# Kernel optimization log

Hardware: AMD Instinct MI355X
Metric: run time of the kernel (lower is better)

Reference implementation:

```python
import jax, jax.numpy as jnp
import numpy as np

N_AGENTS = 8

def _nearest(x, codebook):
    # x: [N, D], codebook: [K, D] -> indices [N]
    # squared L2 distance via expansion; argmin over codebook axis
    d2 = (jnp.sum(x * x, axis=1, keepdims=True)
          - 2.0 * x @ codebook.T
          + jnp.sum(codebook * codebook, axis=1)[None, :])  # [N, K]
    return jnp.argmin(d2, axis=1)

def setup_inputs() -> dict:
    key = jax.random.key(0)
    ks = jax.random.split(key, 16)
    s = 0.02
    H, D_in, R, K, S = 512, 256, 64, 256, 512
    inp = {
        "inputs": jax.random.normal(ks[0], (131072, D_in), jnp.float32),
        "W0": jax.random.normal(ks[1], (D_in, H), jnp.float32) * s,
        "b0": jnp.zeros((H,), jnp.float32),
        "W1": jax.random.normal(ks[2], (H, H), jnp.float32) * s,
        "b1": jnp.zeros((H,), jnp.float32),
        "W2": jax.random.normal(ks[3], (H, R), jnp.float32) * s,
        "b2": jnp.zeros((R,), jnp.float32),
        "codebook": jax.random.normal(ks[4], (K, R), jnp.float32),
        "W3": jax.random.normal(ks[5], (R, H), jnp.float32) * s,
        "b3": jnp.zeros((H,), jnp.float32),
        "W4": jax.random.normal(ks[6], (N_AGENTS * H, H), jnp.float32) * s,
        "b4": jnp.zeros((H,), jnp.float32),
        "W5": jax.random.normal(ks[7], (H, S), jnp.float32) * s,
        "b5": jnp.zeros((S,), jnp.float32),
    }
    return inp

def reference(inputs, W0, b0, W1, b1, W2, b2, codebook, W3, b3, W4, b4, W5, b5):
    # encode: fc2(relu(fc1(relu(fc0(x)))))
    h = jax.nn.relu(inputs @ W0 + b0)
    h = jax.nn.relu(h @ W1 + b1)
    z_e = h @ W2 + b2  # [N, role_dim]

    # emb(z_e, weight_sg=True): straight-through to z_e, codebook detached
    idx1 = _nearest(z_e, codebook)
    z_q_raw = jnp.take(codebook, idx1, axis=0)
    z_q = z_e + jax.lax.stop_gradient(z_q_raw - z_e)

    # emb(z_e.detach()): grad flows to codebook only (gather -> scatter-add vjp)
    z_e_sg = jax.lax.stop_gradient(z_e)
    idx2 = _nearest(z_e_sg, codebook)
    role_emb = jnp.take(codebook, idx2, axis=0)

    # decode
    rec = jax.nn.relu(z_q @ W3 + b3).reshape(-1, N_AGENTS * W3.shape[1])
    rec = jax.nn.relu(rec @ W4 + b4)
    recon = rec @ W5 + b5  # [N/n_agents, state_dim]
    return recon, z_e, role_emb
```

## Files before the change

kernel.cpp:

```cpp
#include <hip/hip_runtime.h>
#include <hip/hip_bf16.h>
#include <cstddef>

__device__ __forceinline__ unsigned short f2bf(float f) {
    union { float f; unsigned int u; } v; v.f = f;
    unsigned int r = (v.u + 0x7fffu + ((v.u >> 16) & 1u)) >> 16;
    return (unsigned short)r;
}

typedef __bf16    bf16x8 __attribute__((ext_vector_type(8)));
typedef float     f32x4  __attribute__((ext_vector_type(4)));
typedef _Float16  f16x8  __attribute__((ext_vector_type(8)));

#define SPLIT_SCALE 2.44140625e-4f

typedef const __attribute__((address_space(1))) void cglb_t;
typedef __attribute__((address_space(3))) void lds_t;

__device__ __forceinline__ void fsplit(float v, _Float16& hi, _Float16& lo) {
    hi = (_Float16)v;
    lo = (_Float16)((v - (float)hi) * 4096.0f);
}

__device__ __forceinline__ int swz4(int r) { return (r & 3) ^ ((r >> 2) & 3); }

template<int K>
__global__ __launch_bounds__(256, 3)
void gemm_split7(const _Float16* __restrict__ Ahi, const _Float16* __restrict__ Alo,
                 const _Float16* __restrict__ Bhi, const _Float16* __restrict__ Blo,
                 const float* __restrict__ bias,
                 _Float16* __restrict__ Chi, _Float16* __restrict__ Clo,
                 int M, int N)
{
    constexpr int BK = 32;
    constexpr int NS = K / BK;

    __shared__ alignas(16) _Float16 SA[2][2][128 * 32];
    __shared__ alignas(16) _Float16 SB[2][2][64 * 32];

    const int tid  = threadIdx.x;
    const int lane = tid & 63;
    const int w    = tid >> 6;

    int bx = blockIdx.x, by = blockIdx.y;
    {
        const int gx = gridDim.x, nwg = gx * gridDim.y;
        if ((nwg & 7) == 0) {
            int d = bx + by * gx;
            int L = (d & 7) * (nwg >> 3) + (d >> 3);
            bx = L % gx; by = L / gx;
        }
    }
    const int bm = by * 128;
    const int bn = bx * 64;

    f32x4 acc0[2][4], acc1[2][4];
#pragma unroll
    for (int m = 0; m < 2; ++m)
#pragma unroll
        for (int n = 0; n < 4; ++n) {
            acc0[m][n] = (f32x4){0.f, 0.f, 0.f, 0.f};
            acc1[m][n] = (f32x4){0.f, 0.f, 0.f, 0.f};
        }

    auto stage = [&](int buf, int k0) {
#pragma unroll
        for (int pl = 0; pl < 2; ++pl) {
            const _Float16* src = pl ? Alo : Ahi;
#pragma unroll
            for (int j = 0; j < 2; ++j) {
                const int p16 = (w * 2 + j) * 64 + lane;
                const int r   = p16 >> 2;
                const int c   = (p16 & 3) ^ swz4(r);
                const _Float16* g = src + (size_t)(bm + r) * K + k0 + c * 8;
                __builtin_amdgcn_global_load_lds((cglb_t*)g,
                    (lds_t*)&SA[buf][pl][p16 * 8], 16, 0, 0);
            }
            const _Float16* srcB = pl ? Blo : Bhi;
            const int p16b = w * 64 + lane;
            const int rb   = p16b >> 2;
            const int cb   = (p16b & 3) ^ swz4(rb);
            const _Float16* gB = srcB + (size_t)(bn + rb) * K + k0 + cb * 8;
            __builtin_amdgcn_global_load_lds((cglb_t*)gB,
                (lds_t*)&SB[buf][pl][p16b * 8], 16, 0, 0);
        }
    };

    stage(0, 0);
    __syncthreads();

    const int g   = lane >> 4;
    const int r15 = lane & 15;

#pragma unroll
    for (int s = 0; s < NS; ++s) {
        const int p = s & 1;
        if (s + 1 < NS) stage(p ^ 1, (s + 1) * BK);

        f16x8 ah[2], al[2];
#pragma unroll
        for (int m = 0; m < 2; ++m) {
            const int R = w * 32 + m * 16 + r15;
            const int a16 = R * 4 + (g ^ swz4(R));
            ah[m] = *reinterpret_cast<const f16x8*>(&SA[p][0][a16 * 8]);
            al[m] = *reinterpret_cast<const f16x8*>(&SA[p][1][a16 * 8]);
        }
#pragma unroll
        for (int n = 0; n < 4; ++n) {
            const int rB = n * 16 + r15;
            const int b16 = rB * 4 + (g ^ swz4(rB));
            const f16x8 bh = *reinterpret_cast<const f16x8*>(&SB[p][0][b16 * 8]);
            const f16x8 bl = *reinterpret_cast<const f16x8*>(&SB[p][1][b16 * 8]);
#pragma unroll
            for (int m = 0; m < 2; ++m)
                acc0[m][n] = __builtin_amdgcn_mfma_f32_16x16x32_f16(
                    ah[m], bh, acc0[m][n], 0, 0, 0);
#pragma unroll
            for (int m = 0; m < 2; ++m)
                acc1[m][n] = __builtin_amdgcn_mfma_f32_16x16x32_f16(
                    ah[m], bl, acc1[m][n], 0, 0, 0);
#pragma unroll
            for (int m = 0; m < 2; ++m)
                acc1[m][n] = __builtin_amdgcn_mfma_f32_16x16x32_f16(
                    al[m], bh, acc1[m][n], 0, 0, 0);
        }
        __syncthreads();
    }

#pragma unroll
    for (int m = 0; m < 2; ++m)
#pragma unroll
        for (int n = 0; n < 4; ++n) {
            const int col = bn + n * 16 + r15;
            const float bv = bias[col];
#pragma unroll
            for (int q = 0; q < 4; ++q) {
                const int row = bm + w * 32 + m * 16 + (lane >> 4) * 4 + q;
                float v = acc0[m][n][q] + SPLIT_SCALE * acc1[m][n][q] + bv;
                v = fmaxf(v, 0.f);
                _Float16 hi, lo; fsplit(v, hi, lo);
                Chi[(size_t)row * N + col] = hi;
                Clo[(size_t)row * N + col] = lo;
            }
        }
}

template<bool RELU, bool OUT_BF16>
__global__ __launch_bounds__(256, 3)
void gemm_bt7(const unsigned short* __restrict__ A,
              const unsigned short* __restrict__ Bt,
              const float* __restrict__ bias,
              void* __restrict__ Cv, int M, int N, int K)
{
    constexpr int BK = 32;

    __shared__ alignas(16) unsigned short SA[2][128 * 32];
    __shared__ alignas(16) unsigned short SB[2][128 * 32];

    const int tid  = threadIdx.x;
    const int lane = tid & 63;
    const int w    = tid >> 6;
    const int wr   = (w >> 1) * 64;
    const int wc   = (w & 1) * 64;

    int bx = blockIdx.x, by = blockIdx.y;
    {
        const int gx = gridDim.x, nwg = gx * gridDim.y;
        if ((nwg & 7) == 0) {
            int d = bx + by * gx;
            int L = (d & 7) * (nwg >> 3) + (d >> 3);
            bx = L % gx; by = L / gx;
        }
    }
    const int bm = by * 128;
    const int bn = bx * 128;

    f32x4 acc[4][4];
#pragma unroll
    for (int m = 0; m < 4; ++m)
#pragma unroll
        for (int n = 0; n < 4; ++n) acc[m][n] = (f32x4){0.f, 0.f, 0.f, 0.f};

    auto stage = [&](int buf, int k0) {
#pragma unroll
        for (int j = 0; j < 2; ++j) {
            const int p16 = (w * 2 + j) * 64 + lane;
            const int r   = p16 >> 2;
            const int c   = (p16 & 3) ^ swz4(r);
            const unsigned short* gA = A + (size_t)(bm + r) * K + k0 + c * 8;
            __builtin_amdgcn_global_load_lds((cglb_t*)gA,
                (lds_t*)&SA[buf][p16 * 8], 16, 0, 0);
            const unsigned short* gB = Bt + (size_t)(bn + r) * K + k0 + c * 8;
            __builtin_amdgcn_global_load_lds((cglb_t*)gB,
                (lds_t*)&SB[buf][p16 * 8], 16, 0, 0);
        }
    };

    stage(0, 0);
    __syncthreads();

    const int g   = lane >> 4;
    const int r15 = lane & 15;
    const int NS  = K / BK;

    for (int s = 0; s < NS; ++s) {
        const int p = s & 1;
        if (s + 1 < NS) stage(p ^ 1, (s + 1) * BK);

        bf16x8 af[4], bf[4];
#pragma unroll
        for (int m = 0; m < 4; ++m) {
            const int R = wr + m * 16 + r15;
            const int a16 = R * 4 + (g ^ swz4(R));
            af[m] = *reinterpret_cast<const bf16x8*>(&SA[p][a16 * 8]);
        }
#pragma unroll
        for (int n = 0; n < 4; ++n) {
            const int RB = wc + n * 16 + r15;
            const int b16 = RB * 4 + (g ^ swz4(RB));
            bf[n] = *reinterpret_cast<const bf16x8*>(&SB[p][b16 * 8]);
        }
#pragma unroll
        for (int m = 0; m < 4; ++m)
#pragma unroll
            for (int n = 0; n < 4; ++n)
                acc[m][n] = __builtin_amdgcn_mfma_f32_16x16x32_bf16(
                    af[m], bf[n], acc[m][n], 0, 0, 0);
        __syncthreads();
    }

#pragma unroll
    for (int m = 0; m < 4; ++m)
#pragma unroll
        for (int n = 0; n < 4; ++n) {
            const int col = bn + wc + n * 16 + r15;
            const float bv = bias[col];
#pragma unroll
            for (int q = 0; q < 4; ++q) {
                const int row = bm + wr + m * 16 + (lane >> 4) * 4 + q;
                float v = acc[m][n][q] + bv;
                if (RELU) v = fmaxf(v, 0.f);
                if (OUT_BF16)
                    reinterpret_cast<unsigned short*>(Cv)[(size_t)row * N + col] = f2bf(v);
                else
                    reinterpret_cast<float*>(Cv)[(size_t)row * N + col] = v;
            }
        }
}

__global__ __launch_bounds__(256)
void gemm_ze_mfma(const _Float16* __restrict__ Ahi, const _Float16* __restrict__ Alo,
                  const _Float16* __restrict__ Bhi, const _Float16* __restrict__ Blo,
                  const float* __restrict__ bias, float* __restrict__ C, int M)
{
    constexpr int K = 512, N = 64;
    const int tid  = threadIdx.x;
    const int lane = tid & 63;
    const int w    = tid >> 6;
    const int wr   = (w >> 1) * 64;
    const int wc   = (w & 1) * 32;
    const int bm   = blockIdx.x * 128;

    f32x4 acc0[4][2], acc1[4][2];
#pragma unroll
    for (int m = 0; m < 4; ++m)
#pragma unroll
        for (int n = 0; n < 2; ++n) {
            acc0[m][n] = (f32x4){0.f, 0.f, 0.f, 0.f};
            acc1[m][n] = (f32x4){0.f, 0.f, 0.f, 0.f};
        }

    const int arow = bm + wr + (lane & 15);
    const int kgrp = (lane >> 4) * 8;

#pragma unroll
    for (int ks = 0; ks < K / 32; ++ks) {
        const int k0 = ks * 32 + kgrp;
        f16x8 ah[4], al[4];
#pragma unroll
        for (int m = 0; m < 4; ++m) {
            const size_t ga = (size_t)(arow + m * 16) * K + k0;
            ah[m] = *reinterpret_cast<const f16x8*>(Ahi + ga);
            al[m] = *reinterpret_cast<const f16x8*>(Alo + ga);
        }
#pragma unroll
        for (int n = 0; n < 2; ++n) {
            const size_t gb = (size_t)(wc + n * 16 + (lane & 15)) * K + k0;
            const f16x8 bh = *reinterpret_cast<const f16x8*>(Bhi + gb);
            const f16x8 bl = *reinterpret_cast<const f16x8*>(Blo + gb);
#pragma unroll
            for (int m = 0; m < 4; ++m)
                acc0[m][n] = __builtin_amdgcn_mfma_f32_16x16x32_f16(
                    ah[m], bh, acc0[m][n], 0, 0, 0);
#pragma unroll
            for (int m = 0; m < 4; ++m)
                acc1[m][n] = __builtin_amdgcn_mfma_f32_16x16x32_f16(
                    ah[m], bl, acc1[m][n], 0, 0, 0);
#pragma unroll
            for (int m = 0; m < 4; ++m)
                acc1[m][n] = __builtin_amdgcn_mfma_f32_16x16x32_f16(
                    al[m], bh, acc1[m][n], 0, 0, 0);
        }
    }

#pragma unroll
    for (int m = 0; m < 4; ++m)
#pragma unroll
        for (int n = 0; n < 2; ++n) {
            const int col = wc + n * 16 + (lane & 15);
            const float bv = bias[col];
#pragma unroll
            for (int q = 0; q < 4; ++q) {
                const int row = bm + wr + m * 16 + (lane >> 4) * 4 + q;
                C[(size_t)row * N + col] = acc0[m][n][q] + SPLIT_SCALE * acc1[m][n][q] + bv;
            }
        }
}

#define VQ_EPS 1e-3f
__global__ __launch_bounds__(512)
void vq_mfma(const float* __restrict__ Z, const float* __restrict__ CB,
             const _Float16* __restrict__ Chi, const _Float16* __restrict__ Clo,
             float* __restrict__ OUT, unsigned short* __restrict__ ZQB)
{
    __shared__ float  ccf[256];
    __shared__ double ccd[256];
    __shared__ float  xxf[128];
    __shared__ double xxd[128];
    __shared__ float  redv[4][128];
    __shared__ int    redi[4][128];
    __shared__ float  bv1s[128];
    __shared__ int    bis[128];
    __shared__ int    cand[128][16];
    __shared__ int    ncand[128];
    __shared__ int    fullflag[128];
    __shared__ int    flaglist[128];
    __shared__ int    nflag;

    const int tid  = threadIdx.x;
    const int lane = tid & 63;
    const int w    = tid >> 6;
    const int wr   = (w >> 2) * 64;
    const int wc   = (w & 3) * 64;
    const int bm   = blockIdx.x * 128;

    if (tid == 0) nflag = 0;
    if (tid < 256) {
        const float4* c4 = reinterpret_cast<const float4*>(CB + (size_t)tid * 64);
        double cc = 0.0;
#pragma unroll
        for (int v = 0; v < 16; ++v) {
            float4 f = c4[v];
            cc = fma((double)f.x, (double)f.x, cc);
            cc = fma((double)f.y, (double)f.y, cc);
            cc = fma((double)f.z, (double)f.z, cc);
            cc = fma((double)f.w, (double)f.w, cc);
        }
        ccd[tid] = cc; ccf[tid] = (float)cc;
    }
    if (tid < 128) {
        const float4* z4 = reinterpret_cast<const float4*>(Z + (size_t)(bm + tid) * 64);
        double xx = 0.0;
#pragma unroll
        for (int v = 0; v < 16; ++v) {
            float4 f = z4[v];
            xx = fma((double)f.x, (double)f.x, xx);
            xx = fma((double)f.y, (double)f.y, xx);
            xx = fma((double)f.z, (double)f.z, xx);
            xx = fma((double)f.w, (double)f.w, xx);
        }
        xxd[tid] = xx; xxf[tid] = (float)xx;
        ncand[tid] = 0; fullflag[tid] = 0;
    }
    __syncthreads();

    f32x4 acc0[4][4], acc1[4][4];
#pragma unroll
    for (int m = 0; m < 4; ++m)
#pragma unroll
        for (int n = 0; n < 4; ++n) {
            acc0[m][n] = (f32x4){0.f, 0.f, 0.f, 0.f};
            acc1[m][n] = (f32x4){0.f, 0.f, 0.f, 0.f};
        }

    const int arow = bm + wr + (lane & 15);
    const int kgrp = (lane >> 4) * 8;

#pragma unroll
    for (int ks = 0; ks < 2; ++ks) {
        const int k0 = ks * 32 + kgrp;
        f16x8 ah[4], al[4];
#pragma unroll
        for (int m = 0; m < 4; ++m) {
            const float* src = Z + (size_t)(arow + m * 16) * 64 + k0;
            float4 v0 = *reinterpret_cast<const float4*>(src);
            float4 v1 = *reinterpret_cast<const float4*>(src + 4);
            float vv[8] = {v0.x, v0.y, v0.z, v0.w, v1.x, v1.y, v1.z, v1.w};
            f16x8 hh, ll;
#pragma unroll
            for (int j = 0; j < 8; ++j) {
                _Float16 hi, lo; fsplit(vv[j], hi, lo);
                hh[j] = hi; ll[j] = lo;
            }
            ah[m] = hh; al[m] = ll;
        }
#pragma unroll
        for (int n = 0; n < 4; ++n) {
            const size_t gb = (size_t)(wc + n * 16 + (lane & 15)) * 64 + k0;
            const f16x8 bh = *reinterpret_cast<const f16x8*>(Chi + gb);
            const f16x8 bl = *reinterpret_cast<const f16x8*>(Clo + gb);
#pragma unroll
            for (int m = 0; m < 4; ++m)
                acc0[m][n] = __builtin_amdgcn_mfma_f32_16x16x32_f16(
                    ah[m], bh, acc0[m][n], 0, 0, 0);
#pragma unroll
            for (int m = 0; m < 4; ++m)
                acc1[m][n] = __builtin_amdgcn_mfma_f32_16x16x32_f16(
                    ah[m], bl, acc1[m][n], 0, 0, 0);
#pragma unroll
            for (int m = 0; m < 4; ++m)
                acc1[m][n] = __builtin_amdgcn_mfma_f32_16x16x32_f16(
                    al[m], bh, acc1[m][n], 0, 0, 0);
        }
    }

#pragma unroll
    for (int m = 0; m < 4; ++m)
#pragma unroll
        for (int n = 0; n < 4; ++n) {
            const int col = wc + n * 16 + (lane & 15);
            const float cf = ccf[col];
#pragma unroll
            for (int q = 0; q < 4; ++q) {
                const int rl = wr + m * 16 + (lane >> 4) * 4 + q;
                float dot = acc0[m][n][q] + SPLIT_SCALE * acc1[m][n][q];
                acc0[m][n][q] = (xxf[rl] - 2.0f * dot) + cf;
            }
        }

    float bvr[4][4]; int bir[4][4];
#pragma unroll
    for (int m = 0; m < 4; ++m)
#pragma unroll
        for (int q = 0; q < 4; ++q) {
            float bv = 3.4e38f; int bi = 0;
#pragma unroll
            for (int n = 0; n < 4; ++n) {
                const int col = wc + n * 16 + (lane & 15);
                const float v = acc0[m][n][q];
                if (v < bv || (v == bv && col < bi)) { bv = v; bi = col; }
            }
            bvr[m][q] = bv; bir[m][q] = bi;
        }
#pragma unroll
    for (int mask = 1; mask < 16; mask <<= 1) {
#pragma unroll
        for (int m = 0; m < 4; ++m)
#pragma unroll
            for (int q = 0; q < 4; ++q) {
                float ov = __shfl_xor(bvr[m][q], mask);
                int   oi = __shfl_xor(bir[m][q], mask);
                if (ov < bvr[m][q] || (ov == bvr[m][q] && oi < bir[m][q])) {
                    bvr[m][q] = ov; bir[m][q] = oi;
                }
            }
    }
    if ((lane & 15) == 0) {
#pragma unroll
        for (int m = 0; m < 4; ++m)
#pragma unroll
            for (int q = 0; q < 4; ++q) {
                const int rl = wr + m * 16 + (lane >> 4) * 4 + q;
                redv[w & 3][rl] = bvr[m][q];
                redi[w & 3][rl] = bir[m][q];
            }
    }
    __syncthreads();

    if (tid < 128) {
        float bv = 3.4e38f; int bi = 0;
#pragma unroll
        for (int nw = 0; nw < 4; ++nw) {
            float v = redv[nw][tid];
            if (v < bv) { bv = v; bi = redi[nw][tid]; }
        }
        bv1s[tid] = bv; bis[tid] = bi;
    }
    __syncthreads();

#pragma unroll
    for (int m = 0; m < 4; ++m)
#pragma unroll
        for (int q = 0; q < 4; ++q) {
            const int rl = wr + m * 16 + (lane >> 4) * 4 + q;
            const float thr = bv1s[rl] + VQ_EPS;
#pragma unroll
            for (int n = 0; n < 4; ++n) {
                const int col = wc + n * 16 + (lane & 15);
                if (acc0[m][n][q] <= thr) {
                    int s = atomicAdd(&ncand[rl], 1);
                    if (s < 16) cand[rl][s] = col;
                    else        fullflag[rl] = 1;
                }
            }
        }
    __syncthreads();

    if (tid < 128) {
        const int nc_ = ncand[tid] < 16 ? ncand[tid] : 16;
        if (nc_ > 1 && !fullflag[tid]) {
            const float4* z4p = reinterpret_cast<const float4*>(Z + (size_t)(bm + tid) * 64);
            const double xx = xxd[tid];
            double best = 1.0e300; int bi = 256;
            for (int s = 0; s < nc_; ++s) {
                const int e = cand[tid][s];
                const float4* c4p = reinterpret_cast<const float4*>(CB + (size_t)e * 64);
                double dot = 0.0;
#pragma unroll
                for (int v = 0; v < 16; ++v) {
                    float4 zf = z4p[v], cf4 = c4p[v];
                    dot = fma((double)zf.x, (double)cf4.x, dot);
                    dot = fma((double)zf.y, (double)cf4.y, dot);
                    dot = fma((double)zf.z, (double)cf4.z, dot);
                    dot = fma((double)zf.w, (double)cf4.w, dot);
                }
                double d2x = (xx - 2.0 * dot) + ccd[e];
                if (d2x < best || (d2x == best && e < bi)) { best = d2x; bi = e; }
            }
            bis[tid] = bi;
        }
        if (fullflag[tid]) {
            int s = atomicAdd(&nflag, 1);
            flaglist[s] = tid;
        }
    }
    __syncthreads();

    for (int fi = w; fi < nflag; fi += 8) {
        const int rl = flaglist[fi];
        const float* zr = Z + (size_t)(bm + rl) * 64;
        const double xx = xxd[rl];
        double best = 1.0e300; int bi = 256;
#pragma unroll
        for (int j = 0; j < 4; ++j) {
            const int e = lane + j * 64;
            const float* c = CB + (size_t)e * 64;
            double dot = 0.0;
#pragma unroll
            for (int d = 0; d < 64; ++d)
                dot = fma((double)zr[d], (double)c[d], dot);
            double d2x = (xx - 2.0 * dot) + ccd[e];
            if (d2x < best || (d2x == best && e < bi)) { best = d2x; bi = e; }
        }
#pragma unroll
        for (int mask = 1; mask < 64; mask <<= 1) {
            double ov = __shfl_xor(best, mask);
            int    oi = __shfl_xor(bi, mask);
            if (ov < best || (ov == best && oi < bi)) { best = ov; bi = oi; }
        }
        if (lane == 0) bis[rl] = bi;
    }
    __syncthreads();

    {
        const int row  = tid >> 2;
        const int part = tid & 3;
        const int bi   = bis[row];
        const float4* src = reinterpret_cast<const float4*>(CB + (size_t)bi * 64) + part * 4;
        float* dst = OUT + (size_t)(bm + row) * 64 + part * 16;
        unsigned short* dq = ZQB + (size_t)(bm + row) * 64 + part * 16;
#pragma unroll
        for (int v = 0; v < 4; ++v) {
            float4 f = src[v];
            *reinterpret_cast<float4*>(dst + v * 4) = f;
            ushort4 qb = { f2bf(f.x), f2bf(f.y), f2bf(f.z), f2bf(f.w) };
            *reinterpret_cast<ushort4*>(dq + v * 4) = qb;
        }
    }
}

__global__ __launch_bounds__(256)
void transpose_bf16(const float* __restrict__ W, unsigned short* __restrict__ Wt,
                    int K, int N)
{
    int idx = blockIdx.x * 256 + threadIdx.x;
    if (idx >= K * N) return;
    int n = idx / K, k = idx % K;
    Wt[idx] = f2bf(W[(size_t)k * N + n]);
}

__global__ __launch_bounds__(256)
void transpose_split_f16(const float* __restrict__ W,
                         _Float16* __restrict__ Whi, _Float16* __restrict__ Wlo,
                         int K, int N)
{
    int idx = blockIdx.x * 256 + threadIdx.x;
    if (idx >= K * N) return;
    int n = idx / K, k = idx % K;
    _Float16 hi, lo; fsplit(W[(size_t)k * N + n], hi, lo);
    Whi[idx] = hi; Wlo[idx] = lo;
}

__global__ __launch_bounds__(256)
void split_vec_f16(const float* __restrict__ src,
                   _Float16* __restrict__ hi, _Float16* __restrict__ lo, long n8)
{
    long i = (long)blockIdx.x * 256 + threadIdx.x;
    if (i >= n8) return;
    float4 a = *reinterpret_cast<const float4*>(&src[i * 8]);
    float4 b = *reinterpret_cast<const float4*>(&src[i * 8 + 4]);
    _Float16 h[8], l[8];
    fsplit(a.x, h[0], l[0]); fsplit(a.y, h[1], l[1]);
    fsplit(a.z, h[2], l[2]); fsplit(a.w, h[3], l[3]);
    fsplit(b.x, h[4], l[4]); fsplit(b.y, h[5], l[5]);
    fsplit(b.z, h[6], l[6]); fsplit(b.w, h[7], l[7]);
    *reinterpret_cast<float4*>(&hi[i * 8]) = *reinterpret_cast<float4*>(h);
    *reinterpret_cast<float4*>(&lo[i * 8]) = *reinterpret_cast<float4*>(l);
}

__global__ __launch_bounds__(256)
void split_flat_f16(const float* __restrict__ src,
                    _Float16* __restrict__ hi, _Float16* __restrict__ lo, int n)
{
    int i = blockIdx.x * 256 + threadIdx.x;
    if (i >= n) return;
    _Float16 h, l; fsplit(src[i], h, l);
    hi[i] = h; lo[i] = l;
}

extern "C" void kernel_launch(void* const* d_in, const int* in_sizes, int n_in,
                              void* d_out, int out_size, void* d_ws, size_t ws_size,
                              hipStream_t stream)
{
    const float* X  = (const float*)d_in[0];
    const float* W0 = (const float*)d_in[1];
    const float* b0 = (const float*)d_in[2];
    const float* W1 = (const float*)d_in[3];
    const float* b1 = (const float*)d_in[4];
    const float* W2 = (const float*)d_in[5];
    const float* b2 = (const float*)d_in[6];
    const float* CB = (const float*)d_in[7];
    const float* W3 = (const float*)d_in[8];
    const float* b3 = (const float*)d_in[9];
    const float* W4 = (const float*)d_in[10];
    const float* b4 = (const float*)d_in[11];
    const float* W5 = (const float*)d_in[12];
    const float* b5 = (const float*)d_in[13];

    const int D_in = 256, H = 512, R = 64, S = 512, NA = 8;
    const int Mtot = in_sizes[0] / D_in;

    float* recon = (float*)d_out;
    float* ze    = recon + (size_t)(Mtot / NA) * S;
    float* remb  = ze + (size_t)Mtot * R;

    char* p = (char*)d_ws;
    _Float16* W0hi = (_Float16*)p;  p += (size_t)H * D_in * 2;
    _Float16* W0lo = (_Float16*)p;  p += (size_t)H * D_in * 2;
    _Float16* W1hi = (_Float16*)p;  p += (size_t)H * H * 2;
    _Float16* W1lo = (_Float16*)p;  p += (size_t)H * H * 2;
    _Float16* W2thi = (_Float16*)p; p += (size_t)R * H * 2;
    _Float16* W2tlo = (_Float16*)p; p += (size_t)R * H * 2;
    _Float16* CBhi = (_Float16*)p;  p += (size_t)256 * R * 2;
    _Float16* CBlo = (_Float16*)p;  p += (size_t)256 * R * 2;
    unsigned short* W3t = (unsigned short*)p;  p += (size_t)H * R * 2;
    unsigned short* W4t = (unsigned short*)p;  p += (size_t)H * (NA * H) * 2;
    unsigned short* W5t = (unsigned short*)p;  p += (size_t)S * H * 2;
    size_t fixed = (size_t)(p - (char*)d_ws);
    fixed = (fixed + 255) & ~(size_t)255;

    int nc = 1;
    while (nc < 128) {
        size_t rpcT = (size_t)Mtot / nc;
        if (fixed + rpcT * 5248 + 1024 <= ws_size) break;
        nc *= 2;
    }
    const int rpc = Mtot / nc;
    char* q = (char*)d_ws + fixed;
    _Float16* Xhi  = (_Float16*)q;                 q += (size_t)rpc * D_in * 2;
    _Float16* Xlo  = (_Float16*)q;                 q += (size_t)rpc * D_in * 2;
    _Float16* h0hi = (_Float16*)q;                 q += (size_t)rpc * H * 2;
    _Float16* h0lo = (_Float16*)q;                 q += (size_t)rpc * H * 2;
    _Float16* h1hi = (_Float16*)q;                 q += (size_t)rpc * H * 2;
    _Float16* h1lo = (_Float16*)q;                 q += (size_t)rpc * H * 2;
    unsigned short* zqb = (unsigned short*)q;      q += (size_t)rpc * R * 2;
    unsigned short* rec1b = (unsigned short*)h0hi;
    unsigned short* rec2b = (unsigned short*)h1hi;

    transpose_split_f16<<<(H * D_in + 255) / 256, 256, 0, stream>>>(W0, W0hi, W0lo, D_in, H);
    transpose_split_f16<<<(H * H + 255) / 256, 256, 0, stream>>>(W1, W1hi, W1lo, H, H);
    transpose_split_f16<<<(H * R + 255) / 256, 256, 0, stream>>>(W2, W2thi, W2tlo, H, R);
    split_flat_f16<<<(256 * R + 255) / 256, 256, 0, stream>>>(CB, CBhi, CBlo, 256 * R);
    transpose_bf16<<<(H * R + 255) / 256, 256, 0, stream>>>(W3, W3t, R, H);
    transpose_bf16<<<(H * NA * H + 255) / 256, 256, 0, stream>>>(W4, W4t, NA * H, H);
    transpose_bf16<<<(S * H + 255) / 256, 256, 0, stream>>>(W5, W5t, H, S);

    for (int r0 = 0; r0 < Mtot; r0 += rpc) {
        const int M6 = rpc / NA;
        split_vec_f16<<<(int)(((long)rpc * D_in / 8 + 255) / 256), 256, 0, stream>>>(
            X + (size_t)r0 * D_in, Xhi, Xlo, (long)rpc * D_in / 8);
        gemm_split7<256><<<dim3(H / 64, rpc / 128), 256, 0, stream>>>(
            Xhi, Xlo, W0hi, W0lo, b0, h0hi, h0lo, rpc, H);
        gemm_split7<512><<<dim3(H / 64, rpc / 128), 256, 0, stream>>>(
            h0hi, h0lo, W1hi, W1lo, b1, h1hi, h1lo, rpc, H);
        gemm_ze_mfma<<<rpc / 128, 256, 0, stream>>>(
            h1hi, h1lo, W2thi, W2tlo, b2, ze + (size_t)r0 * R, rpc);
        vq_mfma<<<rpc / 128, 512, 0, stream>>>(
            ze + (size_t)r0 * R, CB, CBhi, CBlo,
            remb + (size_t)r0 * R, zqb);
        gemm_bt7<true, true><<<dim3(H / 128, rpc / 128), 256, 0, stream>>>(
            zqb, W3t, b3, rec1b, rpc, H, R);
        gemm_bt7<true, true><<<dim3(H / 128, M6 / 128), 256, 0, stream>>>(
            rec1b, W4t, b4, rec2b, M6, H, NA * H);
        gemm_bt7<false, false><<<dim3(S / 128, M6 / 128), 256, 0, stream>>>(
            rec2b, W5t, b5, recon + (size_t)(r0 / NA) * S, M6, S, H);
    }
}
```

Baseline: 951.6 us.

## Split encoder and decoder into separate chunk loops with overlapping workspace regions

Stores the quantized z_q for all rows in the fixed workspace and reuses workspace regions A/B between encoder intermediates and decoder buffers. This cuts the per-row workspace cost, so fewer chunks (larger rpc) fit. The decoder then runs in its own loop with chunks twice as large as the encoder's. Fewer, larger launches are meant to reduce launch overhead and improve GPU fill for the small decoder GEMMs (M6 = rows/8), at the cost of extra aliasing complexity.

```diff
diff --git a/kernel.cpp b/kernel.cpp
--- a/kernel.cpp
+++ b/kernel.cpp
@@ -666,26 +666,31 @@
     unsigned short* W3t = (unsigned short*)p;  p += (size_t)H * R * 2;
     unsigned short* W4t = (unsigned short*)p;  p += (size_t)H * (NA * H) * 2;
     unsigned short* W5t = (unsigned short*)p;  p += (size_t)S * H * 2;
+    unsigned short* zqb = (unsigned short*)p;  p += (size_t)Mtot * R * 2;
     size_t fixed = (size_t)(p - (char*)d_ws);
     fixed = (fixed + 255) & ~(size_t)255;
 
     int nc = 1;
     while (nc < 128) {
         size_t rpcT = (size_t)Mtot / nc;
-        if (fixed + rpcT * 5248 + 1024 <= ws_size) break;
+        if (fixed + rpcT * 4096 + 1024 <= ws_size) break;
         nc *= 2;
     }
     const int rpc = Mtot / nc;
-    char* q = (char*)d_ws + fixed;
-    _Float16* Xhi  = (_Float16*)q;                 q += (size_t)rpc * D_in * 2;
-    _Float16* Xlo  = (_Float16*)q;                 q += (size_t)rpc * D_in * 2;
-    _Float16* h0hi = (_Float16*)q;                 q += (size_t)rpc * H * 2;
-    _Float16* h0lo = (_Float16*)q;                 q += (size_t)rpc * H * 2;
-    _Float16* h1hi = (_Float16*)q;                 q += (size_t)rpc * H * 2;
-    _Float16* h1lo = (_Float16*)q;                 q += (size_t)rpc * H * 2;
-    unsigned short* zqb = (unsigned short*)q;      q += (size_t)rpc * R * 2;
-    unsigned short* rec1b = (unsigned short*)h0hi;
-    unsigned short* rec2b = (unsigned short*)h1hi;
+    char* regionA = (char*)d_ws + fixed;
+    char* regionB = regionA + (size_t)rpc * 2048;
+
+    _Float16* Xhi  = (_Float16*)regionA;
+    _Float16* Xlo  = Xhi + (size_t)rpc * D_in;
+    _Float16* h1hi = (_Float16*)regionA;
+    _Float16* h1lo = h1hi + (size_t)rpc * H;
+    _Float16* h0hi = (_Float16*)regionB;
+    _Float16* h0lo = h0hi + (size_t)rpc * H;
+
+    int dc = (nc >= 2) ? nc / 2 : 1;
+    const int Mdec = Mtot / dc;
+    unsigned short* rec1b = (unsigned short*)regionB;
+    unsigned short* rec2b = (unsigned short*)regionA;
 
     transpose_split_f16<<<(H * D_in + 255) / 256, 256, 0, stream>>>(W0, W0hi, W0lo, D_in, H);
     transpose_split_f16<<<(H * H + 255) / 256, 256, 0, stream>>>(W1, W1hi, W1lo, H, H);
@@ -696,7 +701,6 @@
     transpose_bf16<<<(S * H + 255) / 256, 256, 0, stream>>>(W5, W5t, H, S);
 
     for (int r0 = 0; r0 < Mtot; r0 += rpc) {
-        const int M6 = rpc / NA;
         split_vec_f16<<<(int)(((long)rpc * D_in / 8 + 255) / 256), 256, 0, stream>>>(
             X + (size_t)r0 * D_in, Xhi, Xlo, (long)rpc * D_in / 8);
         gemm_split7<256><<<dim3(H / 64, rpc / 128), 256, 0, stream>>>(
@@ -707,9 +711,13 @@
             h1hi, h1lo, W2thi, W2tlo, b2, ze + (size_t)r0 * R, rpc);
         vq_mfma<<<rpc / 128, 512, 0, stream>>>(
             ze + (size_t)r0 * R, CB, CBhi, CBlo,
-            remb + (size_t)r0 * R, zqb);
-        gemm_bt7<true, true><<<dim3(H / 128, rpc / 128), 256, 0, stream>>>(
-            zqb, W3t, b3, rec1b, rpc, H, R);
+            remb + (size_t)r0 * R, zqb + (size_t)r0 * R);
+    }
+
+    for (int r0 = 0; r0 < Mtot; r0 += Mdec) {
+        const int M6 = Mdec / NA;
+        gemm_bt7<true, true><<<dim3(H / 128, Mdec / 128), 256, 0, stream>>>(
+            zqb + (size_t)r0 * R, W3t, b3, rec1b, Mdec, H, R);
         gemm_bt7<true, true><<<dim3(H / 128, M6 / 128), 256, 0, stream>>>(
             rec1b, W4t, b4, rec2b, M6, H, NA * H);
         gemm_bt7<false, false><<<dim3(S / 128, M6 / 128), 256, 0, stream>>>(
```

Result: faster. 842.3 us (median of 2 runs) (-11.5%).
